# Kernel optimization log

Hardware: AMD Instinct MI355X
Metric: run time of the kernel (lower is better)

Reference implementation:

```python
import jax, jax.numpy as jnp
import numpy as np

GRID_H, GRID_W, INPUT_DIM = 256, 256, 64
BATCH = 4096


def setup_inputs() -> dict:
    key = jax.random.key(0)
    k_in, k_w = jax.random.split(key)
    inputs = jax.random.uniform(k_in, (BATCH, INPUT_DIM), dtype=jnp.float32)
    # SOM weights initialized uniform[0,1) as in the original layer
    weights_map = jax.random.uniform(k_w, (GRID_H, GRID_W, INPUT_DIM), dtype=jnp.float32)
    return {"inputs": inputs, "weights_map": weights_map}


def reference(inputs, weights_map):
    """Inference forward of SOM2dLayer: find BMU coords + quantization error.

    inputs:      [B, D]
    weights_map: [H, W, D]
    returns (bmu_indices [B,2] int32, quantization_errors [B] float32)
    """
    H, W, D = weights_map.shape
    flat_w = weights_map.reshape(H * W, D)            # [N, D]
    x2 = jnp.sum(inputs * inputs, axis=1, keepdims=True)      # [B, 1]
    w2 = jnp.sum(flat_w * flat_w, axis=1)                     # [N]
    d2 = x2 - 2.0 * (inputs @ flat_w.T) + w2                  # [B, N]
    d2 = jnp.maximum(d2, 0.0)                                 # numerical floor
    bmu_flat = jnp.argmin(d2, axis=1)                         # [B]
    bmu_y = (bmu_flat // W).astype(jnp.int32)
    bmu_x = (bmu_flat % W).astype(jnp.int32)
    bmu_indices = jnp.stack([bmu_y, bmu_x], axis=1)           # [B, 2]
    min_d2 = jnp.take_along_axis(d2, bmu_flat[:, None], axis=1)[:, 0]
    quantization_errors = jnp.sqrt(min_d2)                    # [B]
    return bmu_indices, quantization_errors
```

## Files before the change

kernel.cpp:

```cpp
#include <hip/hip_runtime.h>
#include <math.h>


typedef short  bf16x8 __attribute__((ext_vector_type(8)));
typedef float  f32x4  __attribute__((ext_vector_type(4)));
typedef unsigned short u16;

constexpr int D     = 64;
constexpr int NW    = 65536;
constexpr int B     = 4096;
constexpr int NSUB  = 256;
constexpr int NFINE = NW / 16;
constexpr float MARG_HALF = 0.15f;

constexpr int STRIPS   = 32;
constexpr int STRIP_N  = NW / STRIPS;
constexpr int ROWS_BLK = 128;
constexpr int WAVE_N   = STRIP_N / 4;

__device__ inline u16 bf16u(float f) {
    union { float f; unsigned u; } v; v.f = f;
    unsigned b = v.u;
    b += 0x7fffu + ((b >> 16) & 1u);
    return (u16)(b >> 16);
}

__device__ inline u16 bf16up(float f) {
    union { float f; unsigned u; } v; v.f = f;
    unsigned h = v.u >> 16;
    if ((v.u & 0xFFFFu) && !(v.u >> 31)) h += 1;
    return (u16)h;
}

__global__ __launch_bounds__(256) void k_prep(const float* __restrict__ w,
                                              const float* __restrict__ x,
                                              u16* __restrict__ whi,
                                              u16* __restrict__ xhi,
                                              float* __restrict__ w2c) {
    const int idx = blockIdx.x * 256 + threadIdx.x;
    if (idx < NW) {
        const float4* wr = reinterpret_cast<const float4*>(w + (size_t)idx * D);
        u16* orow = whi + (size_t)idx * D;
        float a0 = 0.f, a1 = 0.f, a2 = 0.f, a3 = 0.f;
#pragma unroll
        for (int h = 0; h < 8; ++h) {
            float4 v0 = wr[2 * h], v1 = wr[2 * h + 1];
            a0 = fmaf(v0.x, v0.x, a0); a1 = fmaf(v0.y, v0.y, a1);
            a2 = fmaf(v0.z, v0.z, a2); a3 = fmaf(v0.w, v0.w, a3);
            a0 = fmaf(v1.x, v1.x, a0); a1 = fmaf(v1.y, v1.y, a1);
            a2 = fmaf(v1.z, v1.z, a2); a3 = fmaf(v1.w, v1.w, a3);
            bf16x8 o = {(short)bf16u(v0.x), (short)bf16u(v0.y),
                        (short)bf16u(v0.z), (short)bf16u(v0.w),
                        (short)bf16u(v1.x), (short)bf16u(v1.y),
                        (short)bf16u(v1.z), (short)bf16u(v1.w)};
            *reinterpret_cast<bf16x8*>(orow + 8 * h) = o;
        }
        w2c[idx] = -0.5f * ((a0 + a1) + (a2 + a3));
    } else {
        const int r = idx - NW;
        const float4* xr = reinterpret_cast<const float4*>(x + (size_t)r * D);
        u16* orow = xhi + (size_t)r * D;
#pragma unroll
        for (int h = 0; h < 8; ++h) {
            float4 v0 = xr[2 * h], v1 = xr[2 * h + 1];
            bf16x8 o = {(short)bf16u(v0.x), (short)bf16u(v0.y),
                        (short)bf16u(v0.z), (short)bf16u(v0.w),
                        (short)bf16u(v1.x), (short)bf16u(v1.y),
                        (short)bf16u(v1.z), (short)bf16u(v1.w)};
            *reinterpret_cast<bf16x8*>(orow + 8 * h) = o;
        }
    }
}

template <int WRITE_FINE>
__global__ __launch_bounds__(256, 2) void k_screen0(
        const u16* __restrict__ whi, const u16* __restrict__ xhi,
        const float* __restrict__ w2c, float* __restrict__ pm,
        u16* __restrict__ pmf) {
    __shared__ __align__(16) u16 fsh[4][2048];
    __shared__ __align__(16) float pmsh[512];
    const int bid   = blockIdx.x;
    const int strip = bid & 31;
    const int rbk   = bid >> 5;
    const int tid   = threadIdx.x;
    const int wv    = tid >> 6;
    const int lane  = tid & 63;
    const int col   = lane & 15;
    const int kg    = lane >> 4;
    const int row0  = rbk * ROWS_BLK;
    const int W0    = strip * STRIP_N + wv * WAVE_N;

    bf16x8 a[8][2];
#pragma unroll
    for (int rg = 0; rg < 8; ++rg)
#pragma unroll
        for (int h = 0; h < 2; ++h)
            a[rg][h] = *reinterpret_cast<const bf16x8*>(
                xhi + (size_t)(row0 + rg * 16 + col) * D + h * 32 + kg * 8);

    float mx[8][4];
#pragma unroll
    for (int rg = 0; rg < 8; ++rg)
#pragma unroll
        for (int r = 0; r < 4; ++r) mx[rg][r] = -3.4e38f;

    for (int ch = 0; ch < 2; ++ch) {
        for (int mo = 0; mo < 8; ++mo) {
#pragma unroll
            for (int mi = 0; mi < 2; ++mi) {
                const int m = ch * 16 + mo * 2 + mi;
                const int n = W0 + m * 16 + col;
                const u16* wp = whi + (size_t)n * D + kg * 8;
                const bf16x8 b0 = *reinterpret_cast<const bf16x8*>(wp);
                const bf16x8 b1 = *reinterpret_cast<const bf16x8*>(wp + 32);
                const float c = w2c[n];
                const f32x4 cq = {c, c, c, c};
#pragma unroll
                for (int rg = 0; rg < 8; ++rg) {
                    f32x4 acc = __builtin_amdgcn_mfma_f32_16x16x32_bf16(a[rg][0], b0, cq, 0, 0, 0);
                    acc = __builtin_amdgcn_mfma_f32_16x16x32_bf16(a[rg][1], b1, acc, 0, 0, 0);
                    mx[rg][0] = fmaxf(mx[rg][0], acc[0]);
                    mx[rg][1] = fmaxf(mx[rg][1], acc[1]);
                    mx[rg][2] = fmaxf(mx[rg][2], acc[2]);
                    mx[rg][3] = fmaxf(mx[rg][3], acc[3]);
                }
            }
        }

        const int s_st = strip * 8 + ch * 4 + wv;

        if (WRITE_FINE) {
            u16* st = &fsh[wv][0];
#pragma unroll
            for (int rg = 0; rg < 8; ++rg)
#pragma unroll
                for (int r = 0; r < 4; ++r)
                    st[(rg * 16 + kg * 4 + r) * 16 + col] = bf16up(mx[rg][r]);
        }

#pragma unroll
        for (int rg = 0; rg < 8; ++rg) {
            float v0 = mx[rg][0], v1 = mx[rg][1], v2 = mx[rg][2], v3 = mx[rg][3];
#pragma unroll
            for (int sh = 1; sh < 16; sh <<= 1) {
                v0 = fmaxf(v0, __shfl_xor(v0, sh, 64));
                v1 = fmaxf(v1, __shfl_xor(v1, sh, 64));
                v2 = fmaxf(v2, __shfl_xor(v2, sh, 64));
                v3 = fmaxf(v3, __shfl_xor(v3, sh, 64));
            }
            float vv = v0;
            vv = (col == 1) ? v1 : vv;
            vv = (col == 2) ? v2 : vv;
            vv = (col == 3) ? v3 : vv;
            if (col < 4)
                pmsh[(rg * 16 + kg * 4 + col) * 4 + wv] = vv;
            mx[rg][0] = -3.4e38f; mx[rg][1] = -3.4e38f;
            mx[rg][2] = -3.4e38f; mx[rg][3] = -3.4e38f;
        }

        if (WRITE_FINE) {
            const char* src = reinterpret_cast<const char*>(&fsh[wv][0]);
            char* dst = (char*)pmf + ((size_t)s_st * 32 + rbk) * 4096;
#pragma unroll
            for (int i = 0; i < 4; ++i)
                *reinterpret_cast<float4*>(dst + i * 1024 + lane * 16) =
                    *reinterpret_cast<const float4*>(src + i * 1024 + lane * 16);
        }

        __syncthreads();
        if (tid < 128) {
            float4 v = *reinterpret_cast<const float4*>(&pmsh[tid * 4]);
            *reinterpret_cast<float4*>(
                &pm[(size_t)(row0 + tid) * NSUB + strip * 8 + ch * 4]) = v;
        }
        __syncthreads();
    }
}

template <int FINE>
__global__ __launch_bounds__(256) void k_rescore(
        const float* __restrict__ x, const float* __restrict__ w,
        const float* __restrict__ w2c, const float* __restrict__ pm,
        const u16* __restrict__ pmf, float* __restrict__ out) {
    const int wv   = threadIdx.x >> 6;
    const int lane = threadIdx.x & 63;
    const int row  = blockIdx.x * 4 + wv;
    const int rbk2 = row >> 7;
    const int rl   = row & 127;

    float pv[4];
#pragma unroll
    for (int it = 0; it < 4; ++it)
        pv[it] = pm[(size_t)row * NSUB + it * 64 + lane];
    float gm = fmaxf(fmaxf(pv[0], pv[1]), fmaxf(pv[2], pv[3]));
#pragma unroll
    for (int s = 1; s < 64; s <<= 1) gm = fmaxf(gm, __shfl_xor(gm, s, 64));
    const float thr = gm - MARG_HALF;

    const float4* xr = reinterpret_cast<const float4*>(x + (size_t)row * D);
    float4 xq[16];
#pragma unroll
    for (int q = 0; q < 16; ++q) xq[q] = xr[q];

    float bestv = 3.4e38f;
    int   besti = 0x7fffffff;

#pragma unroll
    for (int it = 0; it < 4; ++it) {
        unsigned long long bm = __ballot(pv[it] >= thr);
        while (bm) {
            int sb = __ffsll(bm) - 1;
            bm &= bm - 1;
            int sub  = it * 64 + sb;
            int base = (sub >> 3) * 2048 + (sub & 3) * 512 + ((sub >> 2) & 1) * 256;

            if (FINE) {
                float fv = -3.4e38f;
                if (lane < 16) {
                    union { unsigned u; float f; } c;
                    c.u = (unsigned)pmf[((size_t)sub * 32 + rbk2) * 2048
                                        + rl * 16 + lane] << 16;
                    fv = c.f;
                }
                unsigned long long fm = __ballot(fv >= thr);
                while (fm) {
                    int colq = __ffsll(fm) - 1;
                    fm &= fm - 1;
                    int j = lane & 15, q = lane >> 4;
                    int n = base + j * 16 + colq;
                    const float4* wr = reinterpret_cast<const float4*>(w + (size_t)n * D);
                    float d0 = 0.f, d1 = 0.f, d2 = 0.f, d3 = 0.f;
#pragma unroll
                    for (int k = 0; k < 4; ++k) {
                        float4 wq = wr[q * 4 + k];
                        float4 xv = xq[q * 4 + k];
                        d0 = fmaf(xv.x, wq.x, d0); d1 = fmaf(xv.y, wq.y, d1);
                        d2 = fmaf(xv.z, wq.z, d2); d3 = fmaf(xv.w, wq.w, d3);
                    }
                    float d = (d0 + d1) + (d2 + d3);
                    d += __shfl_xor(d, 16, 64);
                    d += __shfl_xor(d, 32, 64);
                    float val = -2.f * (d + w2c[n]);
                    if (val < bestv || (val == bestv && n < besti)) { bestv = val; besti = n; }
                }
            } else {
#pragma unroll
                for (int p4 = 0; p4 < 4; ++p4) {
                    int n = base + p4 * 64 + lane;
                    const float4* wr = reinterpret_cast<const float4*>(w + (size_t)n * D);
                    float d0 = 0.f, d1 = 0.f, d2 = 0.f, d3 = 0.f;
#pragma unroll
                    for (int q = 0; q < 16; ++q) {
                        float4 wq = wr[q];
                        d0 = fmaf(xq[q].x, wq.x, d0);
                        d1 = fmaf(xq[q].y, wq.y, d1);
                        d2 = fmaf(xq[q].z, wq.z, d2);
                        d3 = fmaf(xq[q].w, wq.w, d3);
                    }
                    float dot = (d0 + d1) + (d2 + d3);
                    float val = -2.f * (dot + w2c[n]);
                    if (val < bestv || (val == bestv && n < besti)) { bestv = val; besti = n; }
                }
            }
        }
    }
#pragma unroll
    for (int s = 1; s < 64; s <<= 1) {
        float ov = __shfl_xor(bestv, s, 64);
        int   oi = __shfl_xor(besti, s, 64);
        if (ov < bestv || (ov == bestv && oi < besti)) { bestv = ov; besti = oi; }
    }
    if (lane == 0) {
        float a0 = 0.f, a1 = 0.f, a2 = 0.f, a3 = 0.f;
#pragma unroll
        for (int q = 0; q < 16; ++q) {
            a0 = fmaf(xq[q].x, xq[q].x, a0);
            a1 = fmaf(xq[q].y, xq[q].y, a1);
            a2 = fmaf(xq[q].z, xq[q].z, a2);
            a3 = fmaf(xq[q].w, xq[q].w, a3);
        }
        float x2 = (a0 + a1) + (a2 + a3);
        float d2f = x2 + bestv;
        if (d2f < 0.f) d2f = 0.f;
        out[row * 2 + 0] = (float)(besti >> 8);
        out[row * 2 + 1] = (float)(besti & 255);
        out[2 * B + row] = sqrtf(d2f);
    }
}

__global__ __launch_bounds__(256) void fb_w2(const float* __restrict__ w,
                                             float* __restrict__ w2) {
    int n = blockIdx.x * 256 + threadIdx.x;
    const float4* wr = reinterpret_cast<const float4*>(w + (size_t)n * D);
    float a0 = 0.f, a1 = 0.f, a2 = 0.f, a3 = 0.f;
#pragma unroll
    for (int q = 0; q < 16; ++q) {
        float4 v = wr[q];
        a0 = fmaf(v.x, v.x, a0); a1 = fmaf(v.y, v.y, a1);
        a2 = fmaf(v.z, v.z, a2); a3 = fmaf(v.w, v.w, a3);
    }
    w2[n] = (a0 + a1) + (a2 + a3);
}

__global__ __launch_bounds__(256) void fb_main(const float* __restrict__ x,
                                               const float* __restrict__ w,
                                               const float* __restrict__ w2,
                                               float* __restrict__ ps,
                                               int* __restrict__ pi) {
    constexpr int NSTRIP = NW / 32;
    const int rb    = blockIdx.x & 15;
    const int strip = blockIdx.x >> 4;
    const int row   = rb * 256 + threadIdx.x;
    float xr[D];
    const float4* xrow = reinterpret_cast<const float4*>(x + (size_t)row * D);
#pragma unroll
    for (int q = 0; q < 16; ++q) {
        float4 v = xrow[q];
        xr[q * 4 + 0] = v.x; xr[q * 4 + 1] = v.y;
        xr[q * 4 + 2] = v.z; xr[q * 4 + 3] = v.w;
    }
    float best = 3.4e38f; int bidx = 0;
    const int n0 = strip * NSTRIP, n1 = n0 + NSTRIP;
    for (int n = n0; n < n1; ++n) {
        const float* wr = w + (size_t)n * D;
        float a0 = 0.f, a1 = 0.f, a2 = 0.f, a3 = 0.f;
#pragma unroll
        for (int d = 0; d < D; d += 4) {
            a0 = fmaf(xr[d + 0], wr[d + 0], a0);
            a1 = fmaf(xr[d + 1], wr[d + 1], a1);
            a2 = fmaf(xr[d + 2], wr[d + 2], a2);
            a3 = fmaf(xr[d + 3], wr[d + 3], a3);
        }
        float s = fmaf(-2.f, (a0 + a1) + (a2 + a3), w2[n]);
        if (s < best) { best = s; bidx = n; }
    }
    ps[(size_t)strip * B + row] = best;
    pi[(size_t)strip * B + row] = bidx;
}

__global__ __launch_bounds__(256) void fb_merge(const float* __restrict__ x,
                                                const float* __restrict__ ps,
                                                const int* __restrict__ pi,
                                                float* __restrict__ out) {
    int row = blockIdx.x * 256 + threadIdx.x;
    float bs = 3.5e38f; int bi = 0;
    for (int t = 0; t < 32; ++t) {
        float s = ps[(size_t)t * B + row];
        int   i = pi[(size_t)t * B + row];
        if (s < bs || (s == bs && i < bi)) { bs = s; bi = i; }
    }
    const float4* xrow = reinterpret_cast<const float4*>(x + (size_t)row * D);
    float a0 = 0.f, a1 = 0.f, a2 = 0.f, a3 = 0.f;
#pragma unroll
    for (int q = 0; q < 16; ++q) {
        float4 v = xrow[q];
        a0 = fmaf(v.x, v.x, a0); a1 = fmaf(v.y, v.y, a1);
        a2 = fmaf(v.z, v.z, a2); a3 = fmaf(v.w, v.w, a3);
    }
    float x2 = (a0 + a1) + (a2 + a3);
    float d2 = x2 + bs;
    if (d2 < 0.f) d2 = 0.f;
    out[row * 2 + 0] = (float)(bi >> 8);
    out[row * 2 + 1] = (float)(bi & 255);
    out[2 * B + row] = sqrtf(d2);
}

extern "C" void kernel_launch(void* const* d_in, const int* in_sizes, int n_in,
                              void* d_out, int out_size, void* d_ws, size_t ws_size,
                              hipStream_t stream) {
    const float* x = (const float*)d_in[0];
    const float* w = (const float*)d_in[1];
    float* out = (float*)d_out;

    const size_t whi_sz = (size_t)NW * D * 2;
    const size_t xhi_sz = (size_t)B * D * 2;
    const size_t w2c_sz = (size_t)NW * 4;
    const size_t pm_sz  = (size_t)B * NSUB * 4;
    const size_t pmf_sz = (size_t)NFINE * B * 2;
    const size_t need_c = whi_sz + xhi_sz + w2c_sz + pm_sz;
    const size_t need_f = need_c + pmf_sz;

    if (ws_size >= need_c) {
        char* p = (char*)d_ws;
        u16*   whi = (u16*)p;   p += whi_sz;
        u16*   xhi = (u16*)p;   p += xhi_sz;
        float* w2c = (float*)p; p += w2c_sz;
        float* pm  = (float*)p; p += pm_sz;
        u16*   pmf = (u16*)p;

        k_prep<<<(NW + B) / 256, 256, 0, stream>>>(w, x, whi, xhi, w2c);
        if (ws_size >= need_f) {
            k_screen0<1><<<STRIPS * (B / ROWS_BLK), 256, 0, stream>>>(whi, xhi, w2c, pm, pmf);
            k_rescore<1><<<B / 4, 256, 0, stream>>>(x, w, w2c, pm, pmf, out);
        } else {
            k_screen0<0><<<STRIPS * (B / ROWS_BLK), 256, 0, stream>>>(whi, xhi, w2c, pm, pmf);
            k_rescore<0><<<B / 4, 256, 0, stream>>>(x, w, w2c, pm, pmf, out);
        }
    } else {
        float* w2 = (float*)d_ws;
        float* ps = w2 + NW;
        int*   pi = (int*)(ps + (size_t)32 * B);
        fb_w2<<<NW / 256, 256, 0, stream>>>(w, w2);
        fb_main<<<16 * 32, 256, 0, stream>>>(x, w, w2, ps, pi);
        fb_merge<<<B / 256, 256, 0, stream>>>(x, ps, pi, out);
    }
}
```

Measured before the change: 121.6 us.

## Split screen kernel into single-wave blocks and store partial maxima transposed

The screening kernel now launches one 64-thread wave per block, each covering a contiguous 512-column range for 128 rows. Previously a 256-thread block had four waves on strided sub-ranges. The partial-max array is written directly to global memory in a transposed [sub][row] layout, which removes the shared-memory staging and both __syncthreads per chunk. The rescore kernel reads the transposed layout and uses a simplified subrange base index. This gives more, smaller blocks with no inter-wave sync, at the cost of less coalesced scalar pm stores and strided pm loads in rescore.

```diff
diff --git a/kernel.cpp b/kernel.cpp
--- a/kernel.cpp
+++ b/kernel.cpp
@@ -13,10 +13,8 @@
 constexpr int NFINE = NW / 16;
 constexpr float MARG_HALF = 0.15f;
 
-constexpr int STRIPS   = 32;
-constexpr int STRIP_N  = NW / STRIPS;
-constexpr int ROWS_BLK = 128;
-constexpr int WAVE_N   = STRIP_N / 4;
+constexpr int NRANGE = 128;
+constexpr int RBKS   = 32;
 
 __device__ inline u16 bf16u(float f) {
     union { float f; unsigned u; } v; v.f = f;
@@ -73,22 +71,19 @@
 }
 
 template <int WRITE_FINE>
-__global__ __launch_bounds__(256, 2) void k_screen0(
+__global__ __launch_bounds__(64, 4) void k_screen0(
         const u16* __restrict__ whi, const u16* __restrict__ xhi,
-        const float* __restrict__ w2c, float* __restrict__ pm,
+        const float* __restrict__ w2c, float* __restrict__ pmt,
         u16* __restrict__ pmf) {
-    __shared__ __align__(16) u16 fsh[4][2048];
-    __shared__ __align__(16) float pmsh[512];
-    const int bid   = blockIdx.x;
-    const int strip = bid & 31;
-    const int rbk   = bid >> 5;
-    const int tid   = threadIdx.x;
-    const int wv    = tid >> 6;
-    const int lane  = tid & 63;
-    const int col   = lane & 15;
-    const int kg    = lane >> 4;
-    const int row0  = rbk * ROWS_BLK;
-    const int W0    = strip * STRIP_N + wv * WAVE_N;
+    __shared__ __align__(16) u16 fsh[2048];
+    const int bid  = blockIdx.x;
+    const int nr   = bid & (NRANGE - 1);
+    const int rbk  = bid >> 7;
+    const int lane = threadIdx.x;
+    const int col  = lane & 15;
+    const int kg   = lane >> 4;
+    const int row0 = rbk * 128;
+    const int W0   = nr * 512;
 
     bf16x8 a[8][2];
 #pragma unroll
@@ -127,15 +122,14 @@
             }
         }
 
-        const int s_st = strip * 8 + ch * 4 + wv;
+        const int sub = nr * 2 + ch;
 
         if (WRITE_FINE) {
-            u16* st = &fsh[wv][0];
 #pragma unroll
             for (int rg = 0; rg < 8; ++rg)
 #pragma unroll
                 for (int r = 0; r < 4; ++r)
-                    st[(rg * 16 + kg * 4 + r) * 16 + col] = bf16up(mx[rg][r]);
+                    fsh[(rg * 16 + kg * 4 + r) * 16 + col] = bf16up(mx[rg][r]);
         }
 
 #pragma unroll
@@ -153,34 +147,26 @@
             vv = (col == 2) ? v2 : vv;
             vv = (col == 3) ? v3 : vv;
             if (col < 4)
-                pmsh[(rg * 16 + kg * 4 + col) * 4 + wv] = vv;
+                pmt[(size_t)sub * B + row0 + rg * 16 + kg * 4 + col] = vv;
             mx[rg][0] = -3.4e38f; mx[rg][1] = -3.4e38f;
             mx[rg][2] = -3.4e38f; mx[rg][3] = -3.4e38f;
         }
 
         if (WRITE_FINE) {
-            const char* src = reinterpret_cast<const char*>(&fsh[wv][0]);
-            char* dst = (char*)pmf + ((size_t)s_st * 32 + rbk) * 4096;
+            const char* src = reinterpret_cast<const char*>(&fsh[0]);
+            char* dst = (char*)pmf + ((size_t)sub * 32 + rbk) * 4096;
 #pragma unroll
             for (int i = 0; i < 4; ++i)
                 *reinterpret_cast<float4*>(dst + i * 1024 + lane * 16) =
                     *reinterpret_cast<const float4*>(src + i * 1024 + lane * 16);
         }
-
-        __syncthreads();
-        if (tid < 128) {
-            float4 v = *reinterpret_cast<const float4*>(&pmsh[tid * 4]);
-            *reinterpret_cast<float4*>(
-                &pm[(size_t)(row0 + tid) * NSUB + strip * 8 + ch * 4]) = v;
-        }
-        __syncthreads();
     }
 }
 
 template <int FINE>
 __global__ __launch_bounds__(256) void k_rescore(
         const float* __restrict__ x, const float* __restrict__ w,
-        const float* __restrict__ w2c, const float* __restrict__ pm,
+        const float* __restrict__ w2c, const float* __restrict__ pmt,
         const u16* __restrict__ pmf, float* __restrict__ out) {
     const int wv   = threadIdx.x >> 6;
     const int lane = threadIdx.x & 63;
@@ -191,7 +177,7 @@
     float pv[4];
 #pragma unroll
     for (int it = 0; it < 4; ++it)
-        pv[it] = pm[(size_t)row * NSUB + it * 64 + lane];
+        pv[it] = pmt[(size_t)(it * 64 + lane) * B + row];
     float gm = fmaxf(fmaxf(pv[0], pv[1]), fmaxf(pv[2], pv[3]));
 #pragma unroll
     for (int s = 1; s < 64; s <<= 1) gm = fmaxf(gm, __shfl_xor(gm, s, 64));
@@ -212,7 +198,7 @@
             int sb = __ffsll(bm) - 1;
             bm &= bm - 1;
             int sub  = it * 64 + sb;
-            int base = (sub >> 3) * 2048 + (sub & 3) * 512 + ((sub >> 2) & 1) * 256;
+            int base = sub * 256;
 
             if (FINE) {
                 float fv = -3.4e38f;
@@ -385,16 +371,16 @@
         u16*   whi = (u16*)p;   p += whi_sz;
         u16*   xhi = (u16*)p;   p += xhi_sz;
         float* w2c = (float*)p; p += w2c_sz;
-        float* pm  = (float*)p; p += pm_sz;
+        float* pmt = (float*)p; p += pm_sz;
         u16*   pmf = (u16*)p;
 
         k_prep<<<(NW + B) / 256, 256, 0, stream>>>(w, x, whi, xhi, w2c);
         if (ws_size >= need_f) {
-            k_screen0<1><<<STRIPS * (B / ROWS_BLK), 256, 0, stream>>>(whi, xhi, w2c, pm, pmf);
-            k_rescore<1><<<B / 4, 256, 0, stream>>>(x, w, w2c, pm, pmf, out);
+            k_screen0<1><<<NRANGE * RBKS, 64, 0, stream>>>(whi, xhi, w2c, pmt, pmf);
+            k_rescore<1><<<B / 4, 256, 0, stream>>>(x, w, w2c, pmt, pmf, out);
         } else {
-            k_screen0<0><<<STRIPS * (B / ROWS_BLK), 256, 0, stream>>>(whi, xhi, w2c, pm, pmf);
-            k_rescore<0><<<B / 4, 256, 0, stream>>>(x, w, w2c, pm, pmf, out);
+            k_screen0<0><<<NRANGE * RBKS, 64, 0, stream>>>(whi, xhi, w2c, pmt, pmf);
+            k_rescore<0><<<B / 4, 256, 0, stream>>>(x, w, w2c, pmt, pmf, out);
         }
     } else {
         float* w2 = (float*)d_ws;
```

Measured after the change: 287.9 us. 2.37x slower.
